# Kernel tuning notes

Hardware: AMD Instinct MI355X
Metric: run time of the kernel (lower is better)

The kernel has to match this reference:

```python
import jax, jax.numpy as jnp
import numpy as np
import math


def _pearson_similarity(f_p, f_ms):
    # f_p: [B,C,H,W]; f_ms: [B,C,h,w] upsampled bilinearly (align_corners=False,
    # matching F.upsample default) to f_p's spatial size.
    B, C, H, W = f_p.shape
    ms = jax.image.resize(f_ms, (B, C, H, W), method='bilinear')
    ms = ms.reshape(B, C, H * W)
    p = f_p.reshape(B, C, H * W)
    ms_d = ms - jnp.mean(ms, axis=2, keepdims=True)
    p_d = p - jnp.mean(p, axis=2, keepdims=True)
    ms_n = jnp.sqrt(jnp.sum(ms_d * ms_d, axis=2))  # [B,C]
    p_n = jnp.sqrt(jnp.sum(p_d * p_d, axis=2))     # [B,C]
    num = jnp.einsum('bik,bjk->bij', ms_d, p_d)    # [B,C,C]
    # NOTE: original divides row i by ms_n[i]*p_n[i]/100 (same index i for both
    # norms, broadcast over j) — reproduced faithfully.
    denom = (ms_n * p_n / 100.0)[:, :, None]
    return num / denom


def _group_select(s_m):
    # Vectorized equivalent of the per-batch unique/group/sort loop.
    B, C, _ = s_m.shape
    max_val = jnp.max(s_m, axis=2)            # [B,C]
    idx = jnp.argmax(s_m, axis=2)             # [B,C] int, values in [0,C)
    mv = jax.nn.softmax(max_val, axis=1)      # nn.Softmax() on 2D -> dim=1
    # one-hot over the value axis: positions grouped by their argmax value
    onehot = idx[:, :, None] == jnp.arange(C)[None, None, :]    # [B,C,C] bool
    group_score = jnp.sum(mv[:, :, None] * onehot, axis=1)      # [B,C]
    present = jnp.any(onehot, axis=1)                           # [B,C]
    # original orders groups by unique value DESCENDING, then sorts by group
    # score descending (stable argsort => ties broken by value descending)
    desc_vals = jnp.arange(C - 1, -1, -1)
    gs = jnp.where(present, group_score, -jnp.inf)[:, desc_vals]  # [B,C]
    order = jnp.argsort(-gs, axis=1)                               # stable
    scores_sorted = jnp.take_along_axis(gs, order, axis=1)
    vals_sorted = desc_vals[order]
    return scores_sorted, vals_sorted, present


def setup_inputs() -> dict:
    key = jax.random.key(0)
    k1, k2 = jax.random.split(key)
    f_p = jax.random.normal(k1, (16, 256, 96, 96), dtype=jnp.float32)
    f_ms = jax.random.normal(k2, (16, 256, 48, 48), dtype=jnp.float32)
    return {"f_p": f_p, "f_ms": f_ms}


def reference(f_p, f_ms):
    s_m = _pearson_similarity(f_p, f_ms)
    scores, vals, present = _group_select(s_m)
    # min_k = ceil(min over batches of #unique groups / 2) -> data-dependent
    # output width of the selection stage (concrete, not jitted here).
    min_k = math.ceil(int(jnp.min(jnp.sum(present, axis=1))) / 2)
    sel_score = scores[:, :min_k]   # [B,k]
    sel_idx = vals[:, :min_k]       # [B,k] channel indices
    B = f_p.shape[0]
    sel_fp = jax.nn.sigmoid(f_p[jnp.arange(B)[:, None], sel_idx])  # [B,k,H,W]
    w = jax.nn.softmax(sel_score, axis=1)[:, :, None, None]        # [B,k,1,1]
    mask = jnp.sum(w * sel_fp, axis=1)[:, None]                    # [B,1,H,W]
    return f_p + f_p * mask
```

## Files before the change

### kernel.cpp

```cpp
#include <hip/hip_runtime.h>
#include <hip/hip_bf16.h>
#include <math.h>
#include <float.h>

constexpr int CB = 16;
constexpr int CC = 256;
constexpr int PH = 96, PW = 96, PHW = 9216;
constexpr int MH = 48, MW = 48, MHW = 2304;
constexpr int GSTEPS = MHW / 32;

typedef __bf16 bf16x8 __attribute__((ext_vector_type(8)));
typedef float f32x4 __attribute__((ext_vector_type(4)));

__device__ __forceinline__ float sigmoidf_(float x) { return 1.f / (1.f + __expf(-x)); }

__device__ __forceinline__ unsigned f2ord(float f) {
  unsigned u = __float_as_uint(f);
  return (u & 0x80000000u) ? ~u : (u | 0x80000000u);
}

__device__ __forceinline__ void split3(float v, unsigned short& h1, unsigned short& h2,
                                       unsigned short& h3) {
  unsigned u1 = __float_as_uint(v) & 0xFFFF0000u;
  float r1 = v - __uint_as_float(u1);
  unsigned u2 = __float_as_uint(r1) & 0xFFFF0000u;
  float r2 = r1 - __uint_as_float(u2);
  h1 = (unsigned short)(u1 >> 16);
  h2 = (unsigned short)(u2 >> 16);
  h3 = (unsigned short)(__float_as_uint(r2) >> 16);
}

__global__ __launch_bounds__(256) void k_stats(const float* __restrict__ fp,
                                               const float* __restrict__ fms,
                                               unsigned short* __restrict__ padjP,
                                               unsigned short* __restrict__ msP,
                                               float* __restrict__ meanp,
                                               float* __restrict__ pn,
                                               float* __restrict__ meanms,
                                               float* __restrict__ msn) {
  __shared__ __align__(16) float smem[MH * PW];
  __shared__ float rs[4], rss[4];
  const int tid = threadIdx.x;
  if (blockIdx.x < 4096) {
    const int bc = blockIdx.x;
    float (*tmp)[PW] = (float(*)[PW])smem;
    const float* img = fp + (size_t)bc * PHW;
    float4 v9[9];
#pragma unroll
    for (int t = 0; t < 9; ++t) v9[t] = ((const float4*)img)[tid + t * 256];
    float s4[4] = {0.f, 0.f, 0.f, 0.f}, ss4[4] = {0.f, 0.f, 0.f, 0.f};
#pragma unroll
    for (int t = 0; t < 8; ++t) {
      const float4 v = v9[t];
      s4[t & 3] += v.x + v.y + v.z + v.w;
      ss4[t & 3] += v.x * v.x + v.y * v.y + v.z * v.z + v.w * v.w;
    }
    {
      const float4 v = v9[8];
      s4[0] += v.x + v.y + v.z + v.w;
      ss4[0] += v.x * v.x + v.y * v.y + v.z * v.z + v.w * v.w;
    }
    float s = (s4[0] + s4[1]) + (s4[2] + s4[3]);
    float ss = (ss4[0] + ss4[1]) + (ss4[2] + ss4[3]);
    for (int off = 32; off; off >>= 1) { s += __shfl_down(s, off); ss += __shfl_down(ss, off); }
    if ((tid & 63) == 0) { rs[tid >> 6] = s; rss[tid >> 6] = ss; }
    for (int idx4 = tid; idx4 < MH * (PW / 4); idx4 += 256) {
      const int u = idx4 / (PW / 4), w4 = (idx4 - u * (PW / 4)) * 4;
      float4 v;
      if (u == 0) {
        float4 a = *(const float4*)&img[w4];
        float4 b = *(const float4*)&img[PW + w4];
        float4 c = *(const float4*)&img[2 * PW + w4];
        v.x = a.x + 0.75f * b.x + 0.25f * c.x;
        v.y = a.y + 0.75f * b.y + 0.25f * c.y;
        v.z = a.z + 0.75f * b.z + 0.25f * c.z;
        v.w = a.w + 0.75f * b.w + 0.25f * c.w;
      } else if (u == MH - 1) {
        float4 a = *(const float4*)&img[(PH - 3) * PW + w4];
        float4 b = *(const float4*)&img[(PH - 2) * PW + w4];
        float4 c = *(const float4*)&img[(PH - 1) * PW + w4];
        v.x = 0.25f * a.x + 0.75f * b.x + c.x;
        v.y = 0.25f * a.y + 0.75f * b.y + c.y;
        v.z = 0.25f * a.z + 0.75f * b.z + c.z;
        v.w = 0.25f * a.w + 0.75f * b.w + c.w;
      } else {
        float4 a = *(const float4*)&img[(2 * u - 1) * PW + w4];
        float4 b = *(const float4*)&img[2 * u * PW + w4];
        float4 c = *(const float4*)&img[(2 * u + 1) * PW + w4];
        float4 d = *(const float4*)&img[(2 * u + 2) * PW + w4];
        v.x = 0.25f * (a.x + d.x) + 0.75f * (b.x + c.x);
        v.y = 0.25f * (a.y + d.y) + 0.75f * (b.y + c.y);
        v.z = 0.25f * (a.z + d.z) + 0.75f * (b.z + c.z);
        v.w = 0.25f * (a.w + d.w) + 0.75f * (b.w + c.w);
      }
      *(float4*)&tmp[u][w4] = v;
    }
    __syncthreads();
    if (tid == 0) {
      float S = rs[0] + rs[1] + rs[2] + rs[3];
      float SS = rss[0] + rss[1] + rss[2] + rss[3];
      meanp[bc] = S / (float)PHW;
      pn[bc] = sqrtf(fmaxf(SS - S * S / (float)PHW, 0.f));
    }
    unsigned short* outp = padjP + (size_t)bc * 3 * MHW;
    for (int idx = tid; idx < MH * (MW / 2); idx += 256) {
      const int u = idx / (MW / 2), j = idx - u * (MW / 2);
      const float* r = tmp[u];
      const int v0 = 2 * j, v1 = 2 * j + 1;
      float val0, val1;
      if (v0 == 0)
        val0 = r[0] + 0.75f * r[1] + 0.25f * r[2];
      else
        val0 = 0.25f * (r[2 * v0 - 1] + r[2 * v0 + 2]) + 0.75f * (r[2 * v0] + r[2 * v0 + 1]);
      if (v1 == MW - 1)
        val1 = 0.25f * r[PW - 3] + 0.75f * r[PW - 2] + r[PW - 1];
      else
        val1 = 0.25f * (r[2 * v1 - 1] + r[2 * v1 + 2]) + 0.75f * (r[2 * v1] + r[2 * v1 + 1]);
      unsigned short a1, a2, a3, b1, b2, b3;
      split3(val0, a1, a2, a3);
      split3(val1, b1, b2, b3);
      const int k = u * MW + v0;
      ushort2 t;
      t.x = a1; t.y = b1; *(ushort2*)&outp[k] = t;
      t.x = a2; t.y = b2; *(ushort2*)&outp[MHW + k] = t;
      t.x = a3; t.y = b3; *(ushort2*)&outp[2 * MHW + k] = t;
    }
  } else {
    const int bc = blockIdx.x - 4096;
    float* m = smem;
    float* t = smem + MHW;
    const float* img = fms + (size_t)bc * MHW;
    float s = 0.f;
    for (int q = tid; q < MHW / 4; q += 256) {
      float4 v = ((const float4*)img)[q];
      ((float4*)m)[q] = v;
      s += v.x + v.y + v.z + v.w;
    }
    for (int off = 32; off; off >>= 1) s += __shfl_down(s, off);
    if ((tid & 63) == 0) rs[tid >> 6] = s;
    __syncthreads();
    const float mean = (rs[0] + rs[1] + rs[2] + rs[3]) / (float)MHW;
    for (int idx = tid; idx < MHW; idx += 256) {
      const int i = idx / MW, j = idx - i * MW;
      const float c = m[idx];
      const float l = (j > 0) ? m[idx - 1] : 0.f;
      const float r = (j < MW - 1) ? m[idx + 1] : 0.f;
      const float dj = (j == 0 || j == MW - 1) ? 1.625f : 1.25f;
      t[idx] = dj * c + 0.375f * (l + r);
    }
    __syncthreads();
    float ss = 0.f;
    for (int idx = tid; idx < MHW; idx += 256) {
      const int i = idx / MW;
      const float c = t[idx];
      const float up = (i > 0) ? t[idx - MW] : 0.f;
      const float dn = (i < MH - 1) ? t[idx + MW] : 0.f;
      const float di = (i == 0 || i == MH - 1) ? 1.625f : 1.25f;
      ss += m[idx] * (di * c + 0.375f * (up + dn));
    }
    for (int off = 32; off; off >>= 1) ss += __shfl_down(ss, off);
    if ((tid & 63) == 0) rss[tid >> 6] = ss;
    __syncthreads();
    if (tid == 0) {
      float SS = rss[0] + rss[1] + rss[2] + rss[3];
      meanms[bc] = mean;
      msn[bc] = sqrtf(fmaxf(SS - (float)PHW * mean * mean, 0.f));
    }
    unsigned short* outp = msP + (size_t)bc * 3 * MHW;
    for (int i4 = tid; i4 < MHW / 4; i4 += 256) {
      const int i = 4 * i4;
      float4 v = *(const float4*)&m[i];
      unsigned short p1[4], p2[4], p3[4];
      split3(v.x, p1[0], p2[0], p3[0]);
      split3(v.y, p1[1], p2[1], p3[1]);
      split3(v.z, p1[2], p2[2], p3[2]);
      split3(v.w, p1[3], p2[3], p3[3]);
      *(ushort4*)&outp[i] = make_ushort4(p1[0], p1[1], p1[2], p1[3]);
      *(ushort4*)&outp[MHW + i] = make_ushort4(p2[0], p2[1], p2[2], p2[3]);
      *(ushort4*)&outp[2 * MHW + i] = make_ushort4(p3[0], p3[1], p3[2], p3[3]);
    }
  }
}

__global__ __launch_bounds__(256) void k_gemm(const unsigned short* __restrict__ msP,
                                              const unsigned short* __restrict__ padjP,
                                              float* __restrict__ dotp) {
  __shared__ unsigned short As[2][2][3][64][40];
  const int n = blockIdx.x;
  const int xcd = n & 7, slot = n >> 3;
  const int b = xcd * 2 + (slot >> 4);
  const int xy = slot & 15;
  const int i0 = (xy >> 2) * 64, j0 = (xy & 3) * 64;
  const int tid = threadIdx.x, lane = tid & 63, wid = tid >> 6;
  const int wr = wid >> 1, wc = wid & 1;
  const int fr = lane & 15, fq = lane >> 4;

  const unsigned short* mats[2] = {
    msP + (size_t)(b * CC + i0) * 3 * MHW,
    padjP + (size_t)(b * CC + j0) * 3 * MHW
  };
  const unsigned short* gsrc[6];
  int lmat[6], lpl[6], lrow[6], lch[6];
#pragma unroll
  for (int q = 0; q < 6; ++q) {
    int t = tid + q * 256;
    int ch = t & 3, pl = (t >> 2) % 3, r128 = t / 12;
    int mat = r128 >> 6, row = r128 & 63;
    gsrc[q] = mats[mat] + ((size_t)row * 3 + pl) * MHW + ch * 8;
    lmat[q] = mat; lpl[q] = pl; lrow[q] = row; lch[q] = ch;
  }
  bf16x8 stg[6];
  f32x4 acc[2][2] = {};

  auto g_load = [&](int kt) {
#pragma unroll
    for (int q = 0; q < 6; ++q) stg[q] = *(const bf16x8*)(gsrc[q] + kt);
  };
  auto l_store = [&](int buf) {
#pragma unroll
    for (int q = 0; q < 6; ++q)
      *(bf16x8*)&As[buf][lmat[q]][lpl[q]][lrow[q]][lch[q] * 8] = stg[q];
  };

  g_load(0);
  l_store(0);
  if (GSTEPS > 1) g_load(32);
  __syncthreads();
  int cur = 0;
  for (int step = 0; step < GSTEPS; ++step) {
    if (step + 1 < GSTEPS) l_store(cur ^ 1);
    if (step + 2 < GSTEPS) g_load((step + 2) * 32);
    bf16x8 af[2][3], bfr[2][3];
#pragma unroll
    for (int ti = 0; ti < 2; ++ti)
#pragma unroll
      for (int p = 0; p < 3; ++p) {
        af[ti][p] = *(const bf16x8*)&As[cur][0][p][wr * 32 + ti * 16 + fr][fq * 8];
        bfr[ti][p] = *(const bf16x8*)&As[cur][1][p][wc * 32 + ti * 16 + fr][fq * 8];
      }
#pragma unroll
    for (int ti = 0; ti < 2; ++ti)
#pragma unroll
      for (int tj = 0; tj < 2; ++tj) {
        f32x4 c = acc[ti][tj];
        c = __builtin_amdgcn_mfma_f32_16x16x32_bf16(af[ti][0], bfr[tj][0], c, 0, 0, 0);
        c = __builtin_amdgcn_mfma_f32_16x16x32_bf16(af[ti][0], bfr[tj][1], c, 0, 0, 0);
        c = __builtin_amdgcn_mfma_f32_16x16x32_bf16(af[ti][1], bfr[tj][0], c, 0, 0, 0);
        c = __builtin_amdgcn_mfma_f32_16x16x32_bf16(af[ti][0], bfr[tj][2], c, 0, 0, 0);
        c = __builtin_amdgcn_mfma_f32_16x16x32_bf16(af[ti][1], bfr[tj][1], c, 0, 0, 0);
        c = __builtin_amdgcn_mfma_f32_16x16x32_bf16(af[ti][2], bfr[tj][0], c, 0, 0, 0);
        acc[ti][tj] = c;
      }
    __syncthreads();
    cur ^= 1;
  }
  float* drow = dotp + ((size_t)b * CC + i0) * CC + j0;
#pragma unroll
  for (int ti = 0; ti < 2; ++ti)
#pragma unroll
    for (int tj = 0; tj < 2; ++tj)
#pragma unroll
      for (int j = 0; j < 4; ++j) {
        int row = wr * 32 + ti * 16 + fq * 4 + j;
        int col = wc * 32 + tj * 16 + fr;
        drow[(size_t)row * CC + col] = acc[ti][tj][j];
      }
}

__global__ __launch_bounds__(256) void k_rowmax(const float* __restrict__ dotp,
                                                const float* __restrict__ meanp,
                                                const float* __restrict__ pn,
                                                const float* __restrict__ meanms,
                                                const float* __restrict__ msn,
                                                float* __restrict__ maxv,
                                                int* __restrict__ amax) {
  const int tid = threadIdx.x;
  const int r = blockIdx.x * 4 + (tid >> 6);
  const int lane = tid & 63;
  const int b = r >> 8;
  const float* d0 = dotp + (size_t)r * CC;
  const float mm = meanms[r];
  const float inv = 100.f / msn[r];
  const int j = lane * 4;
  float4 v0 = *(const float4*)(d0 + j);
  float4 mp4 = *(const float4*)(meanp + b * CC + j);
  float4 pn4 = *(const float4*)(pn + b * CC + j);
  float sv[4];
  sv[0] = (v0.x - (float)PHW * mm * mp4.x) * inv / pn4.x;
  sv[1] = (v0.y - (float)PHW * mm * mp4.y) * inv / pn4.y;
  sv[2] = (v0.z - (float)PHW * mm * mp4.z) * inv / pn4.z;
  sv[3] = (v0.w - (float)PHW * mm * mp4.w) * inv / pn4.w;
  float best = sv[0]; int bj = j;
#pragma unroll
  for (int t = 1; t < 4; ++t)
    if (sv[t] > best) { best = sv[t]; bj = j + t; }
  for (int off = 32; off; off >>= 1) {
    float ov = __shfl_down(best, off);
    int oi = __shfl_down(bj, off);
    if (ov > best || (ov == best && oi < bj)) { best = ov; bj = oi; }
  }
  if (lane == 0) { maxv[r] = best; amax[r] = bj; }
}

__global__ __launch_bounds__(256) void k_group(const float* __restrict__ maxv,
                                               const int* __restrict__ amax,
                                               float* __restrict__ sscore,
                                               int* __restrict__ svals,
                                               int* __restrict__ cnt) {
  const int b = blockIdx.x, tid = threadIdx.x;
  __shared__ float mv[CC];
  __shared__ int sidx[CC];
  __shared__ float gsc[CC];
  __shared__ int pres[CC];
  __shared__ unsigned long long keys[CC];
  __shared__ float r1[4], r2[4];
  __shared__ int r3[4];
  float v = maxv[b * CC + tid];
  sidx[tid] = amax[b * CC + tid];
  float m = v;
  for (int off = 32; off; off >>= 1) m = fmaxf(m, __shfl_down(m, off));
  if ((tid & 63) == 0) r1[tid >> 6] = m;
  __syncthreads();
  float mt = fmaxf(fmaxf(r1[0], r1[1]), fmaxf(r1[2], r1[3]));
  float e = __expf(v - mt);
  float s = e;
  for (int off = 32; off; off >>= 1) s += __shfl_down(s, off);
  if ((tid & 63) == 0) r2[tid >> 6] = s;
  __syncthreads();
  float st = r2[0] + r2[1] + r2[2] + r2[3];
  mv[tid] = e / st;
  __syncthreads();
  float g = 0.f; int p = 0;
  for (int i2 = 0; i2 < CC; ++i2)
    if (sidx[i2] == tid) { g += mv[i2]; p = 1; }
  gsc[tid] = g; pres[tid] = p;
  int pc = p;
  for (int off = 32; off; off >>= 1) pc += __shfl_down(pc, off);
  if ((tid & 63) == 0) r3[tid >> 6] = pc;
  __syncthreads();
  if (tid == 0) cnt[b] = r3[0] + r3[1] + r3[2] + r3[3];
  int c = 255 - tid;
  float val = pres[c] ? gsc[c] : -INFINITY;
  keys[tid] = ((unsigned long long)f2ord(val) << 32) | (unsigned)c;
  __syncthreads();
  for (int ksz = 2; ksz <= 256; ksz <<= 1) {
    for (int jj = ksz >> 1; jj > 0; jj >>= 1) {
      int ixj = tid ^ jj;
      if (ixj > tid) {
        unsigned long long a = keys[tid], o = keys[ixj];
        bool descBlock = ((tid & ksz) == 0);
        bool sw = descBlock ? (a < o) : (a > o);
        if (sw) { keys[tid] = o; keys[ixj] = a; }
      }
      __syncthreads();
    }
  }
  unsigned long long kk = keys[tid];
  int cc2 = (int)(kk & 0xFFFFFFFFull);
  float vv = pres[cc2] ? gsc[cc2] : -INFINITY;
  sscore[b * CC + tid] = vv;
  svals[b * CC + tid] = cc2;
}

__global__ __launch_bounds__(128) void k_wsel(const float* __restrict__ sscore,
                                              const int* __restrict__ cnt,
                                              float* __restrict__ wgt,
                                              int* __restrict__ minkp) {
  const int b = blockIdx.x, tid = threadIdx.x;
  int mn = 0x7fffffff;
#pragma unroll
  for (int t = 0; t < CB; ++t) mn = min(mn, cnt[t]);
  const int mink = (mn + 1) >> 1;
  if (b == 0 && tid == 0) *minkp = mink;
  __shared__ float sh1[2], sh2[2];
  float v = (tid < mink) ? sscore[b * CC + tid] : -INFINITY;
  float m = v;
  for (int off = 32; off; off >>= 1) m = fmaxf(m, __shfl_down(m, off));
  if ((tid & 63) == 0) sh1[tid >> 6] = m;
  __syncthreads();
  float mt = fmaxf(sh1[0], sh1[1]);
  float e = (tid < mink) ? __expf(v - mt) : 0.f;
  float s = e;
  for (int off = 32; off; off >>= 1) s += __shfl_down(s, off);
  if ((tid & 63) == 0) sh2[tid >> 6] = s;
  __syncthreads();
  float st = sh2[0] + sh2[1];
  if (tid < mink) wgt[b * 128 + tid] = e / st;
}

__global__ __launch_bounds__(256) void k_maskout(const float* __restrict__ fp,
                                                 const float* __restrict__ wgt,
                                                 const int* __restrict__ svals,
                                                 const int* __restrict__ minkp,
                                                 float* __restrict__ out) {
  const int b = blockIdx.y;
  const int pos = threadIdx.x & 15;
  const int kq = threadIdx.x >> 4;
  const int hw4 = blockIdx.x * 16 + pos;
  const int mink = *minkp;
  const int qlo = (mink * kq) >> 4, qhi = (mink * (kq + 1)) >> 4;
  const float* base = fp + (size_t)b * CC * PHW;
  float4 acc = make_float4(0.f, 0.f, 0.f, 0.f);
  int k = qlo;
  for (; k + 4 <= qhi; k += 4) {
    float4 vv[4]; float wk[4];
#pragma unroll
    for (int t = 0; t < 4; ++t) {
      int c = svals[b * CC + k + t];
      wk[t] = wgt[b * 128 + k + t];
      vv[t] = ((const float4*)(base + (size_t)c * PHW))[hw4];
    }
#pragma unroll
    for (int t = 0; t < 4; ++t) {
      acc.x += wk[t] * sigmoidf_(vv[t].x);
      acc.y += wk[t] * sigmoidf_(vv[t].y);
      acc.z += wk[t] * sigmoidf_(vv[t].z);
      acc.w += wk[t] * sigmoidf_(vv[t].w);
    }
  }
  for (; k < qhi; ++k) {
    int c = svals[b * CC + k];
    float wk = wgt[b * 128 + k];
    float4 v = ((const float4*)(base + (size_t)c * PHW))[hw4];
    acc.x += wk * sigmoidf_(v.x);
    acc.y += wk * sigmoidf_(v.y);
    acc.z += wk * sigmoidf_(v.z);
    acc.w += wk * sigmoidf_(v.w);
  }
  __shared__ __align__(16) float4 sh[16][16];
  __shared__ __align__(16) float4 msh[16];
  sh[kq][pos] = acc;
  __syncthreads();
  if (kq == 0) {
    float4 r = sh[0][pos];
#pragma unroll
    for (int t = 1; t < 16; ++t) {
      float4 a = sh[t][pos];
      r.x += a.x; r.y += a.y; r.z += a.z; r.w += a.w;
    }
    msh[pos] = r;
  }
  __syncthreads();
  const float4 mk = msh[pos];
  float* outb = out + (size_t)b * CC * PHW;
#pragma unroll
  for (int half = 0; half < 2; ++half) {
    float4 v[8];
#pragma unroll
    for (int j = 0; j < 8; ++j) {
      const int c = (half * 8 + j) * 16 + kq;
      v[j] = ((const float4*)(base + (size_t)c * PHW))[hw4];
    }
#pragma unroll
    for (int j = 0; j < 8; ++j) {
      const int c = (half * 8 + j) * 16 + kq;
      float4 o;
      o.x = v[j].x * (1.f + mk.x);
      o.y = v[j].y * (1.f + mk.y);
      o.z = v[j].z * (1.f + mk.z);
      o.w = v[j].w * (1.f + mk.w);
      ((float4*)(outb + (size_t)c * PHW))[hw4] = o;
    }
  }
}

extern "C" void kernel_launch(void* const* d_in, const int* in_sizes, int n_in,
                              void* d_out, int out_size, void* d_ws, size_t ws_size,
                              hipStream_t stream) {
  (void)in_sizes; (void)n_in; (void)out_size;
  const float* fp = (const float*)d_in[0];
  const float* fms = (const float*)d_in[1];
  float* out = (float*)d_out;

  unsigned short* padjP = (unsigned short*)out;
  unsigned short* msP = (unsigned short*)(out + (size_t)14155776);
  float* dotp = out + (size_t)28311552;

  if (ws_size < (size_t)183000 * 4) return;
  float* wsf = (float*)d_ws;
  float* meanp = wsf;
  float* pnv = wsf + 4096;
  float* meanms = wsf + 8192;
  float* msn = wsf + 12288;
  float* maxv = wsf + 16384;
  float* ssc = wsf + 20480;
  float* wgt = wsf + 24576;
  int* amax = (int*)(wsf + 174080);
  int* sv = (int*)(wsf + 178176);
  int* cntp = (int*)(wsf + 182272);
  int* minkp = (int*)(wsf + 182288);

  k_stats<<<8192, 256, 0, stream>>>(fp, fms, padjP, msP, meanp, pnv, meanms, msn);
  k_gemm<<<256, 256, 0, stream>>>(msP, padjP, dotp);
  k_rowmax<<<(CB * CC) / 4, 256, 0, stream>>>(dotp, meanp, pnv, meanms, msn, maxv, amax);
  k_group<<<CB, 256, 0, stream>>>(maxv, amax, ssc, sv, cntp);
  k_wsel<<<CB, 128, 0, stream>>>(ssc, cntp, wgt, minkp);
  k_maskout<<<dim3(PHW / 4 / 16, CB), 256, 0, stream>>>(fp, wgt, sv, minkp, out);
}
```

Measured before the change: 225.1 us.

## Fuse row-max into group kernel and fold p-stats into downsample loop

The stats kernel no longer makes a separate full-image pass to compute sum and sum of squares. It accumulates them from rows already loaded during the vertical downsample, since rows 2u and 2u+1 together cover every pixel once. The row-max/argmax kernel is merged into the grouping kernel, which removes one launch and the intermediate buffers. The cost is that each thread in the 16-block select kernel now scans a full 256-element row serially with strided per-thread reads, which lowers parallelism for that stage.

```diff
diff --git a/kernel.cpp b/kernel.cpp
--- a/kernel.cpp
+++ b/kernel.cpp
@@ -45,28 +45,10 @@
     const int bc = blockIdx.x;
     float (*tmp)[PW] = (float(*)[PW])smem;
     const float* img = fp + (size_t)bc * PHW;
-    float4 v9[9];
-#pragma unroll
-    for (int t = 0; t < 9; ++t) v9[t] = ((const float4*)img)[tid + t * 256];
-    float s4[4] = {0.f, 0.f, 0.f, 0.f}, ss4[4] = {0.f, 0.f, 0.f, 0.f};
-#pragma unroll
-    for (int t = 0; t < 8; ++t) {
-      const float4 v = v9[t];
-      s4[t & 3] += v.x + v.y + v.z + v.w;
-      ss4[t & 3] += v.x * v.x + v.y * v.y + v.z * v.z + v.w * v.w;
-    }
-    {
-      const float4 v = v9[8];
-      s4[0] += v.x + v.y + v.z + v.w;
-      ss4[0] += v.x * v.x + v.y * v.y + v.z * v.z + v.w * v.w;
-    }
-    float s = (s4[0] + s4[1]) + (s4[2] + s4[3]);
-    float ss = (ss4[0] + ss4[1]) + (ss4[2] + ss4[3]);
-    for (int off = 32; off; off >>= 1) { s += __shfl_down(s, off); ss += __shfl_down(ss, off); }
-    if ((tid & 63) == 0) { rs[tid >> 6] = s; rss[tid >> 6] = ss; }
+    float s = 0.f, ss = 0.f;
     for (int idx4 = tid; idx4 < MH * (PW / 4); idx4 += 256) {
       const int u = idx4 / (PW / 4), w4 = (idx4 - u * (PW / 4)) * 4;
-      float4 v;
+      float4 v, p0, p1;
       if (u == 0) {
         float4 a = *(const float4*)&img[w4];
         float4 b = *(const float4*)&img[PW + w4];
@@ -75,6 +57,7 @@
         v.y = a.y + 0.75f * b.y + 0.25f * c.y;
         v.z = a.z + 0.75f * b.z + 0.25f * c.z;
         v.w = a.w + 0.75f * b.w + 0.25f * c.w;
+        p0 = a; p1 = b;
       } else if (u == MH - 1) {
         float4 a = *(const float4*)&img[(PH - 3) * PW + w4];
         float4 b = *(const float4*)&img[(PH - 2) * PW + w4];
@@ -83,6 +66,7 @@
         v.y = 0.25f * a.y + 0.75f * b.y + c.y;
         v.z = 0.25f * a.z + 0.75f * b.z + c.z;
         v.w = 0.25f * a.w + 0.75f * b.w + c.w;
+        p0 = b; p1 = c;
       } else {
         float4 a = *(const float4*)&img[(2 * u - 1) * PW + w4];
         float4 b = *(const float4*)&img[2 * u * PW + w4];
@@ -92,9 +76,15 @@
         v.y = 0.25f * (a.y + d.y) + 0.75f * (b.y + c.y);
         v.z = 0.25f * (a.z + d.z) + 0.75f * (b.z + c.z);
         v.w = 0.25f * (a.w + d.w) + 0.75f * (b.w + c.w);
+        p0 = b; p1 = c;
       }
+      s += (p0.x + p0.y + p0.z + p0.w) + (p1.x + p1.y + p1.z + p1.w);
+      ss += (p0.x * p0.x + p0.y * p0.y + p0.z * p0.z + p0.w * p0.w) +
+            (p1.x * p1.x + p1.y * p1.y + p1.z * p1.z + p1.w * p1.w);
       *(float4*)&tmp[u][w4] = v;
     }
+    for (int off = 32; off; off >>= 1) { s += __shfl_down(s, off); ss += __shfl_down(ss, off); }
+    if ((tid & 63) == 0) { rs[tid >> 6] = s; rss[tid >> 6] = ss; }
     __syncthreads();
     if (tid == 0) {
       float S = rs[0] + rs[1] + rs[2] + rs[3];
@@ -267,46 +257,14 @@
       }
 }
 
-__global__ __launch_bounds__(256) void k_rowmax(const float* __restrict__ dotp,
+__global__ __launch_bounds__(256) void k_select(const float* __restrict__ dotp,
                                                 const float* __restrict__ meanp,
                                                 const float* __restrict__ pn,
                                                 const float* __restrict__ meanms,
                                                 const float* __restrict__ msn,
-                                                float* __restrict__ maxv,
-                                                int* __restrict__ amax) {
-  const int tid = threadIdx.x;
-  const int r = blockIdx.x * 4 + (tid >> 6);
-  const int lane = tid & 63;
-  const int b = r >> 8;
-  const float* d0 = dotp + (size_t)r * CC;
-  const float mm = meanms[r];
-  const float inv = 100.f / msn[r];
-  const int j = lane * 4;
-  float4 v0 = *(const float4*)(d0 + j);
-  float4 mp4 = *(const float4*)(meanp + b * CC + j);
-  float4 pn4 = *(const float4*)(pn + b * CC + j);
-  float sv[4];
-  sv[0] = (v0.x - (float)PHW * mm * mp4.x) * inv / pn4.x;
-  sv[1] = (v0.y - (float)PHW * mm * mp4.y) * inv / pn4.y;
-  sv[2] = (v0.z - (float)PHW * mm * mp4.z) * inv / pn4.z;
-  sv[3] = (v0.w - (float)PHW * mm * mp4.w) * inv / pn4.w;
-  float best = sv[0]; int bj = j;
-#pragma unroll
-  for (int t = 1; t < 4; ++t)
-    if (sv[t] > best) { best = sv[t]; bj = j + t; }
-  for (int off = 32; off; off >>= 1) {
-    float ov = __shfl_down(best, off);
-    int oi = __shfl_down(bj, off);
-    if (ov > best || (ov == best && oi < bj)) { best = ov; bj = oi; }
-  }
-  if (lane == 0) { maxv[r] = best; amax[r] = bj; }
-}
-
-__global__ __launch_bounds__(256) void k_group(const float* __restrict__ maxv,
-                                               const int* __restrict__ amax,
-                                               float* __restrict__ sscore,
-                                               int* __restrict__ svals,
-                                               int* __restrict__ cnt) {
+                                                float* __restrict__ sscore,
+                                                int* __restrict__ svals,
+                                                int* __restrict__ cnt) {
   const int b = blockIdx.x, tid = threadIdx.x;
   __shared__ float mv[CC];
   __shared__ int sidx[CC];
@@ -315,8 +273,28 @@
   __shared__ unsigned long long keys[CC];
   __shared__ float r1[4], r2[4];
   __shared__ int r3[4];
-  float v = maxv[b * CC + tid];
-  sidx[tid] = amax[b * CC + tid];
+  const int r = b * CC + tid;
+  const float* d0 = dotp + (size_t)r * CC;
+  const float mm = meanms[r];
+  const float inv = 100.f / msn[r];
+  const float* mpb = meanp + b * CC;
+  const float* pnb = pn + b * CC;
+  float best = -INFINITY; int bj = 0;
+  for (int j4 = 0; j4 < CC / 4; ++j4) {
+    float4 v0 = ((const float4*)d0)[j4];
+    float4 mp4 = ((const float4*)mpb)[j4];
+    float4 pn4 = ((const float4*)pnb)[j4];
+    float sv[4];
+    sv[0] = (v0.x - (float)PHW * mm * mp4.x) * inv / pn4.x;
+    sv[1] = (v0.y - (float)PHW * mm * mp4.y) * inv / pn4.y;
+    sv[2] = (v0.z - (float)PHW * mm * mp4.z) * inv / pn4.z;
+    sv[3] = (v0.w - (float)PHW * mm * mp4.w) * inv / pn4.w;
+#pragma unroll
+    for (int t = 0; t < 4; ++t)
+      if (sv[t] > best) { best = sv[t]; bj = j4 * 4 + t; }
+  }
+  const float v = best;
+  sidx[tid] = bj;
   float m = v;
   for (int off = 32; off; off >>= 1) m = fmaxf(m, __shfl_down(m, off));
   if ((tid & 63) == 0) r1[tid >> 6] = m;
@@ -482,18 +460,15 @@
   float* pnv = wsf + 4096;
   float* meanms = wsf + 8192;
   float* msn = wsf + 12288;
-  float* maxv = wsf + 16384;
   float* ssc = wsf + 20480;
   float* wgt = wsf + 24576;
-  int* amax = (int*)(wsf + 174080);
   int* sv = (int*)(wsf + 178176);
   int* cntp = (int*)(wsf + 182272);
   int* minkp = (int*)(wsf + 182288);
 
   k_stats<<<8192, 256, 0, stream>>>(fp, fms, padjP, msP, meanp, pnv, meanms, msn);
   k_gemm<<<256, 256, 0, stream>>>(msP, padjP, dotp);
-  k_rowmax<<<(CB * CC) / 4, 256, 0, stream>>>(dotp, meanp, pnv, meanms, msn, maxv, amax);
-  k_group<<<CB, 256, 0, stream>>>(maxv, amax, ssc, sv, cntp);
+  k_select<<<CB, 256, 0, stream>>>(dotp, meanp, pnv, meanms, msn, ssc, sv, cntp);
   k_wsel<<<CB, 128, 0, stream>>>(ssc, cntp, wgt, minkp);
   k_maskout<<<dim3(PHW / 4 / 16, CB), 256, 0, stream>>>(fp, wgt, sv, minkp, out);
 }
```

Result: faster. 219.2 us (-2.6%).
